# Kernel tuning notes

Hardware: AMD Instinct MI355X
Metric: run time of the kernel (lower is better)

Reference implementation:

```python
import jax, jax.numpy as jnp
import numpy as np

N, D_IN, D_OUT = 16384, 64, 64
AVG_DEG = 32.0
L2_EPS = 1e-12  # torch F.normalize default eps


def setup_inputs() -> dict:
    key = jax.random.key(0)
    kx, ka, kw, kb = jax.random.split(key, 4)
    X = jax.random.normal(kx, (N, D_IN), dtype=jnp.float32)
    # binary adjacency with avg degree ~AVG_DEG (module treats adj as 0/1 mask)
    adj = (jax.random.uniform(ka, (N, N)) < (AVG_DEG / N)).astype(jnp.float32)
    # nn.Linear(2*D_IN, D_OUT): store W as (2*D_IN, D_OUT) for x @ W + b
    bound = 1.0 / np.sqrt(2 * D_IN)
    W = jax.random.uniform(kw, (2 * D_IN, D_OUT), dtype=jnp.float32, minval=-bound, maxval=bound)
    b = jax.random.uniform(kb, (D_OUT,), dtype=jnp.float32, minval=-bound, maxval=bound)
    return {"X": X, "adj": adj, "W": W, "b": b}


def reference(X, adj, W, b):
    # eval-mode mean aggregation: h_neigh = (adj + I) @ X / clamp(rowsum(adj + I), 1)
    # (adj + I) @ X == adj @ X + X, avoiding materializing the NxN identity.
    deg = jnp.clip(jnp.sum(adj, axis=1, keepdims=True) + 1.0, 1.0, None)  # (N,1)
    h_neigh = (adj @ X + X) / deg                                          # (N,D)
    concat = jnp.concatenate([X, h_neigh], axis=1)                         # (N,2D)
    z = concat @ W + b                                                     # (N,O)
    out = jax.nn.relu(z)
    norm = jnp.linalg.norm(out, axis=1, keepdims=True)
    return out / jnp.maximum(norm, L2_EPS)
```

## Files before the change

### kernel.cpp

```cpp
#include <hip/hip_runtime.h>
#include <stdint.h>


#define NROWS  16384
#define DDIM   64
#define MAXNNZ 256

__global__ __launch_bounds__(256) void sage_fused(
    const float* __restrict__ X,
    const float* __restrict__ adj,
    const float* __restrict__ W,
    const float* __restrict__ bias,
    float* __restrict__ out)
{
    __shared__ float sW[128 * 64];
    __shared__ float scat[128];
    __shared__ float spart[4][64];
    __shared__ float sb[64];
    __shared__ int   slist[MAXNNZ];
    __shared__ int   scnt;

    const int tid = threadIdx.x;
    const int row = blockIdx.x;
    const int d   = tid & 63;
    const int g   = tid >> 6;

    if (tid == 0) scnt = 0;

    const uint4* rowp = reinterpret_cast<const uint4*>(adj + (size_t)row * NROWS);
    uint4 v[16];
#pragma unroll
    for (int it = 0; it < 16; ++it) v[it] = rowp[it * 256 + tid];

    {
        const float4* wp  = reinterpret_cast<const float4*>(W);
        float4*       swp = reinterpret_cast<float4*>(sW);
#pragma unroll
        for (int it = 0; it < 8; ++it) swp[it * 256 + tid] = wp[it * 256 + tid];
        if (tid < 64) sb[tid] = bias[tid];
    }
    __syncthreads();

#pragma unroll
    for (int it = 0; it < 16; ++it) {
        const uint4 vv = v[it];
        if (vv.x | vv.y | vv.z | vv.w) {
            const int base = (it * 256 + tid) * 4;
            const uint32_t w4[4] = { vv.x, vv.y, vv.z, vv.w };
#pragma unroll
            for (int j = 0; j < 4; ++j) {
                if (w4[j]) {
                    const int p = atomicAdd(&scnt, 1);
                    if (p < MAXNNZ) slist[p] = base + j;
                }
            }
        }
    }
    __syncthreads();
    const int nnz = min(scnt, MAXNNZ);

    float acc = 0.0f;
    for (int k = g; k < nnz; k += 4) {
        const int j = slist[k];
        acc += X[(size_t)j * DDIM + d];
    }
    spart[g][d] = acc;
    __syncthreads();

    if (tid < 64) {
        const float xi  = X[(size_t)row * DDIM + d];
        const float hs  = spart[0][d] + spart[1][d] + spart[2][d] + spart[3][d] + xi;
        const float deg = (float)scnt + 1.0f;
        scat[d]        = xi;
        scat[DDIM + d] = hs / deg;
    }
    __syncthreads();

    float zp = 0.0f;
#pragma unroll
    for (int kk = 0; kk < 32; ++kk) {
        const int k = (g << 5) + kk;
        zp = fmaf(scat[k], sW[k * 64 + d], zp);
    }
    spart[g][d] = zp;
    __syncthreads();

    if (tid < 64) {
        float z = sb[d] + spart[0][d] + spart[1][d] + spart[2][d] + spart[3][d];
        z = fmaxf(z, 0.0f);
        float s = z * z;
#pragma unroll
        for (int off = 32; off >= 1; off >>= 1) s += __shfl_xor(s, off);
        const float inv = 1.0f / fmaxf(sqrtf(s), 1e-12f);
        out[(size_t)row * DDIM + d] = z * inv;
    }
}

extern "C" void kernel_launch(void* const* d_in, const int* in_sizes, int n_in,
                              void* d_out, int out_size, void* d_ws, size_t ws_size,
                              hipStream_t stream) {
    const float* X   = (const float*)d_in[0];
    const float* adj = (const float*)d_in[1];
    const float* W   = (const float*)d_in[2];
    const float* b   = (const float*)d_in[3];
    float* out = (float*)d_out;
    sage_fused<<<NROWS, 256, 0, stream>>>(X, adj, W, b, out);
}
```

Before: 1.348 ms.

## Assign one wavefront per row with persistent blocks and double-buffered nontemporal adjacency loads

```diff
diff --git a/kernel.cpp b/kernel.cpp
--- a/kernel.cpp
+++ b/kernel.cpp
@@ -2,97 +2,110 @@
 #include <stdint.h>
 
 
-#define NROWS  16384
-#define DDIM   64
-#define MAXNNZ 256
+#define NROWS   16384
+#define DDIM    64
+#define MAXNNZ  256
+#define NBLOCKS 2048
+#define TOTAL_WAVES (NBLOCKS * 4)
+#define ROWS_PER_WAVE (NROWS / TOTAL_WAVES)
 
-__global__ __launch_bounds__(256) void sage_fused(
+typedef uint32_t u32x4 __attribute__((ext_vector_type(4)));
+
+__global__ __launch_bounds__(256, 4) void sage_fused(
     const float* __restrict__ X,
     const float* __restrict__ adj,
     const float* __restrict__ W,
     const float* __restrict__ bias,
     float* __restrict__ out)
 {
-    __shared__ float sW[128 * 64];
-    __shared__ float scat[128];
-    __shared__ float spart[4][64];
-    __shared__ float sb[64];
-    __shared__ int   slist[MAXNNZ];
-    __shared__ int   scnt;
+    __shared__ int   slist[4][MAXNNZ];
+    __shared__ int   scnt[4];
+    __shared__ float scat[4][2 * DDIM];
 
-    const int tid = threadIdx.x;
-    const int row = blockIdx.x;
-    const int d   = tid & 63;
-    const int g   = tid >> 6;
+    const int tid  = threadIdx.x;
+    const int lane = tid & 63;
+    const int w    = tid >> 6;
+    const int gw   = blockIdx.x * 4 + w;
 
-    if (tid == 0) scnt = 0;
+    const float bv = bias[lane];
 
-    const uint4* rowp = reinterpret_cast<const uint4*>(adj + (size_t)row * NROWS);
-    uint4 v[16];
+    for (int r = 0; r < ROWS_PER_WAVE; ++r) {
+        const int row = gw + r * TOTAL_WAVES;
+
+        if (lane == 0) scnt[w] = 0;
+        __builtin_amdgcn_wave_barrier();
+
+        const u32x4* rowp = reinterpret_cast<const u32x4*>(adj + (size_t)row * NROWS);
+        u32x4 c[4], n[4];
 #pragma unroll
-    for (int it = 0; it < 16; ++it) v[it] = rowp[it * 256 + tid];
+        for (int q = 0; q < 4; ++q)
+            c[q] = __builtin_nontemporal_load(&rowp[q * 64 + lane]);
 
-    {
-        const float4* wp  = reinterpret_cast<const float4*>(W);
-        float4*       swp = reinterpret_cast<float4*>(sW);
+#pragma unroll 1
+        for (int s = 0; s < 16; ++s) {
+            if (s < 15) {
 #pragma unroll
-        for (int it = 0; it < 8; ++it) swp[it * 256 + tid] = wp[it * 256 + tid];
-        if (tid < 64) sb[tid] = bias[tid];
-    }
-    __syncthreads();
-
+                for (int q = 0; q < 4; ++q)
+                    n[q] = __builtin_nontemporal_load(&rowp[(s + 1) * 256 + q * 64 + lane]);
+            }
 #pragma unroll
-    for (int it = 0; it < 16; ++it) {
-        const uint4 vv = v[it];
-        if (vv.x | vv.y | vv.z | vv.w) {
-            const int base = (it * 256 + tid) * 4;
-            const uint32_t w4[4] = { vv.x, vv.y, vv.z, vv.w };
+            for (int q = 0; q < 4; ++q) {
+                const u32x4 vv = c[q];
+                if (vv.x | vv.y | vv.z | vv.w) {
+                    const int base = (s * 256 + q * 64 + lane) * 4;
+                    const uint32_t w4[4] = { vv.x, vv.y, vv.z, vv.w };
 #pragma unroll
-            for (int j = 0; j < 4; ++j) {
-                if (w4[j]) {
-                    const int p = atomicAdd(&scnt, 1);
-                    if (p < MAXNNZ) slist[p] = base + j;
+                    for (int j = 0; j < 4; ++j) {
+                        if (w4[j]) {
+                            const int p = atomicAdd(&scnt[w], 1);
+                            if (p < MAXNNZ) slist[w][p] = base + j;
+                        }
+                    }
                 }
             }
+#pragma unroll
+            for (int q = 0; q < 4; ++q) c[q] = n[q];
         }
-    }
-    __syncthreads();
-    const int nnz = min(scnt, MAXNNZ);
+        __builtin_amdgcn_wave_barrier();
 
-    float acc = 0.0f;
-    for (int k = g; k < nnz; k += 4) {
-        const int j = slist[k];
-        acc += X[(size_t)j * DDIM + d];
-    }
-    spart[g][d] = acc;
-    __syncthreads();
+        const int nnz = scnt[w];
+        const int cn  = (nnz < MAXNNZ) ? nnz : MAXNNZ;
 
-    if (tid < 64) {
-        const float xi  = X[(size_t)row * DDIM + d];
-        const float hs  = spart[0][d] + spart[1][d] + spart[2][d] + spart[3][d] + xi;
-        const float deg = (float)scnt + 1.0f;
-        scat[d]        = xi;
-        scat[DDIM + d] = hs / deg;
-    }
-    __syncthreads();
+        float acc = 0.0f;
+        int k = 0;
+        for (; k + 4 <= cn; k += 4) {
+            const int j0 = slist[w][k], j1 = slist[w][k + 1];
+            const int j2 = slist[w][k + 2], j3 = slist[w][k + 3];
+            const float a0 = X[(size_t)j0 * DDIM + lane];
+            const float a1 = X[(size_t)j1 * DDIM + lane];
+            const float a2 = X[(size_t)j2 * DDIM + lane];
+            const float a3 = X[(size_t)j3 * DDIM + lane];
+            acc += (a0 + a1) + (a2 + a3);
+        }
+        for (; k < cn; ++k) acc += X[(size_t)slist[w][k] * DDIM + lane];
 
-    float zp = 0.0f;
+        const float xi = X[(size_t)row * DDIM + lane];
+        const float h  = (acc + xi) / ((float)nnz + 1.0f);
+        scat[w][lane]        = xi;
+        scat[w][DDIM + lane] = h;
+        __builtin_amdgcn_wave_barrier();
+
+        float z0 = bv, z1 = 0.0f, z2 = 0.0f, z3 = 0.0f;
+#pragma unroll 8
+        for (int kk = 0; kk < 2 * DDIM; kk += 4) {
+            z0 = fmaf(scat[w][kk + 0], W[(kk + 0) * DDIM + lane], z0);
+            z1 = fmaf(scat[w][kk + 1], W[(kk + 1) * DDIM + lane], z1);
+            z2 = fmaf(scat[w][kk + 2], W[(kk + 2) * DDIM + lane], z2);
+            z3 = fmaf(scat[w][kk + 3], W[(kk + 3) * DDIM + lane], z3);
+        }
+        float z = (z0 + z1) + (z2 + z3);
+        z = fmaxf(z, 0.0f);
+
+        float s2 = z * z;
 #pragma unroll
-    for (int kk = 0; kk < 32; ++kk) {
-        const int k = (g << 5) + kk;
-        zp = fmaf(scat[k], sW[k * 64 + d], zp);
-    }
-    spart[g][d] = zp;
-    __syncthreads();
-
-    if (tid < 64) {
-        float z = sb[d] + spart[0][d] + spart[1][d] + spart[2][d] + spart[3][d];
-        z = fmaxf(z, 0.0f);
-        float s = z * z;
-#pragma unroll
-        for (int off = 32; off >= 1; off >>= 1) s += __shfl_xor(s, off);
-        const float inv = 1.0f / fmaxf(sqrtf(s), 1e-12f);
-        out[(size_t)row * DDIM + d] = z * inv;
+        for (int off = 32; off >= 1; off >>= 1) s2 += __shfl_xor(s2, off);
+        const float inv = 1.0f / fmaxf(sqrtf(s2), 1e-12f);
+        out[(size_t)row * DDIM + lane] = z * inv;
     }
 }
 
@@ -104,5 +117,5 @@
     const float* W   = (const float*)d_in[2];
     const float* b   = (const float*)d_in[3];
     float* out = (float*)d_out;
-    sage_fused<<<NROWS, 256, 0, stream>>>(X, adj, W, b, out);
+    sage_fused<<<NBLOCKS, 256, 0, stream>>>(X, adj, W, b, out);
 }
```

Result: no change. 1.337 ms (-0.8%).
